# Kernel tuning notes

Measured on AMD Instinct MI355X. Metric: run time of the kernel, lower is better.

Reference implementation:

```python
import jax, jax.numpy as jnp
import numpy as np

H = 16  # num heads
EPS = 1e-5


def layer_norm(x, g, b):
    mu = jnp.mean(x, axis=-1, keepdims=True)
    var = jnp.var(x, axis=-1, keepdims=True)
    return (x - mu) * jax.lax.rsqrt(var + EPS) * g + b


def setup_inputs() -> dict:
    key = jax.random.key(0)
    ks = jax.random.split(key, 8)
    B, T, D, TE = 4, 4096, 1024, 1024
    s = 0.02  # weight init scale
    return {
        "x": jax.random.normal(ks[0], (B, T, D), jnp.float32),
        "emb": jax.random.normal(ks[1], (B, 1, TE), jnp.float32),
        "gate_msa": jax.random.normal(ks[2], (B, 1, D), jnp.float32),
        "norm_g": jnp.ones((D,), jnp.float32),
        "norm_b": jnp.zeros((D,), jnp.float32),
        "Wq": jax.random.normal(ks[3], (D, D), jnp.float32) * s,
        "bq": jnp.zeros((D,), jnp.float32),
        "Wk": jax.random.normal(ks[4], (D, D), jnp.float32) * s,
        "bk": jnp.zeros((D,), jnp.float32),
        "Wv": jax.random.normal(ks[5], (D, D), jnp.float32) * s,
        "bv": jnp.zeros((D,), jnp.float32),
        "emb_W": jax.random.normal(ks[6], (TE, 2 * D), jnp.float32) * s,
        "emb_b": jnp.zeros((2 * D,), jnp.float32),
        "sn_g": jnp.ones((D,), jnp.float32),
        "sn_b": jnp.zeros((D,), jnp.float32),
        "out_W": jax.random.normal(ks[7], (D, D), jnp.float32) * s,
        "out_b": jnp.zeros((D,), jnp.float32),
    }


def reference(x, emb, gate_msa, norm_g, norm_b, Wq, bq, Wk, bk, Wv, bv,
              emb_W, emb_b, sn_g, sn_b, out_W, out_b):
    B, T, D = x.shape
    dh = D // H
    xn = layer_norm(x, norm_g, norm_b)
    q = (xn @ Wq + bq).reshape(B, T, H, dh)
    k = (xn @ Wk + bk).reshape(B, T, H, dh)
    v = (xn @ Wv + bv).reshape(B, T, H, dh)
    q = jax.nn.softmax(q, axis=-1)      # feature-dim softmax
    k = jax.nn.softmax(k, axis=1)       # temporal softmax
    ctx = jnp.einsum('bnhd,bnhl->bhdl', k, v)  # [B,H,dh,dh] context
    y = jnp.einsum('bnhd,bhdl->bnhl', q, ctx).reshape(B, T, D)
    # StylizationBlock (dropout=0 eval semantics)
    emb_out = jax.nn.silu(emb) @ emb_W + emb_b        # [B,1,2D]
    scale, shift = jnp.split(emb_out, 2, axis=-1)
    h = layer_norm(y, sn_g, sn_b) * (1.0 + scale) + shift
    h = jax.nn.silu(h) @ out_W + out_b
    return x + gate_msa * h
```

## Files before the change

kernel.cpp:

```cpp
#include <hip/hip_runtime.h>
#include <stdint.h>

typedef unsigned short u16;
typedef float f32x4 __attribute__((ext_vector_type(4)));
typedef __bf16 bf16x8 __attribute__((ext_vector_type(8)));

__device__ __forceinline__ float b2f(u16 u) {
    union { unsigned int i; float f; } w; w.i = ((unsigned int)u) << 16; return w.f;
}
__device__ __forceinline__ u16 f2b(float f) {
    union { float f; unsigned int i; } w; w.f = f;
    unsigned int r = w.i + 0x7fffu + ((w.i >> 16) & 1u);
    return (u16)(r >> 16);
}
__device__ __forceinline__ void gload16(const void* g, void* l) {
    __builtin_amdgcn_global_load_lds(
        (const __attribute__((address_space(1))) unsigned int*)g,
        (__attribute__((address_space(3))) unsigned int*)l, 16, 0, 0);
}

__global__ __launch_bounds__(256) void prep_k(
    const float* __restrict__ Wq, const float* __restrict__ Wk, const float* __restrict__ Wv,
    const float* __restrict__ Wo, const float* __restrict__ bq, const float* __restrict__ bk,
    const float* __restrict__ bv, const float* __restrict__ ob,
    u16* __restrict__ WqkvT, u16* __restrict__ WoT, float* __restrict__ biasAll,
    float* __restrict__ zeroBase)
{
    int bz = blockIdx.x, tid = threadIdx.x;
    if (bz < 4096) {
        int z = bz >> 10, rem = bz & 1023;
        const float* src = (z == 0) ? Wq : (z == 1) ? Wk : (z == 2) ? Wv : Wo;
        u16* dst = (z < 3) ? (WqkvT + (size_t)z * 1024 * 1024) : WoT;
        __shared__ u16 tile[32][33];
        int tx = tid & 31, ty = tid >> 5;
        int n0 = (rem & 31) * 32, k0 = (rem >> 5) * 32;
#pragma unroll
        for (int i = 0; i < 4; i++) tile[ty + 8 * i][tx] = f2b(src[(size_t)(k0 + ty + 8 * i) * 1024 + n0 + tx]);
        __syncthreads();
#pragma unroll
        for (int i = 0; i < 4; i++) dst[(size_t)(n0 + ty + 8 * i) * 1024 + k0 + tx] = tile[tx][ty + 8 * i];
    } else if (bz < 4112) {
        int i = (bz - 4096) * 256 + tid;
        float v;
        if (i < 1024) v = bq[i];
        else if (i < 2048) v = bk[i - 1024];
        else if (i < 3072) v = bv[i - 2048];
        else v = ob[i - 3072];
        biasAll[i] = v;
    } else {
        int e = (bz - 4112) * 256 + tid;
        ((float4*)zeroBase)[e] = make_float4(0.f, 0.f, 0.f, 0.f);
    }
}

__global__ __launch_bounds__(256) void ln_x(
    const float* __restrict__ x, const float* __restrict__ g, const float* __restrict__ bt,
    u16* __restrict__ xn)
{
    int row = blockIdx.x, tid = threadIdx.x;
    const float* xr = x + (size_t)row * 1024;
    float4 u = *(const float4*)(xr + tid * 4);
    float v0 = u.x, v1 = u.y, v2 = u.z, v3 = u.w;
    float s = v0 + v1 + v2 + v3;
    float s2 = v0 * v0 + v1 * v1 + v2 * v2 + v3 * v3;
#pragma unroll
    for (int m = 32; m > 0; m >>= 1) { s += __shfl_xor(s, m, 64); s2 += __shfl_xor(s2, m, 64); }
    __shared__ float red[8];
    int w = tid >> 6, lane = tid & 63;
    if (lane == 0) { red[w] = s; red[4 + w] = s2; }
    __syncthreads();
    s = red[0] + red[1] + red[2] + red[3];
    s2 = red[4] + red[5] + red[6] + red[7];
    float mean = s * (1.f / 1024.f);
    float var = s2 * (1.f / 1024.f) - mean * mean;
    float rstd = rsqrtf(var + 1e-5f);
    int c = tid * 4;
    float4 gg = *(const float4*)(g + c);
    float4 bb = *(const float4*)(bt + c);
    ushort4 o;
    o.x = f2b((v0 - mean) * rstd * gg.x + bb.x);
    o.y = f2b((v1 - mean) * rstd * gg.y + bb.y);
    o.z = f2b((v2 - mean) * rstd * gg.z + bb.z);
    o.w = f2b((v3 - mean) * rstd * gg.w + bb.w);
    *(ushort4*)(xn + (size_t)row * 1024 + c) = o;
}

__global__ __launch_bounds__(256) void gemm128(
    const u16* __restrict__ A, const u16* __restrict__ Bt, const float* __restrict__ bias,
    int mode, u16* __restrict__ Qb, u16* __restrict__ Kb, u16* __restrict__ Vb,
    float* __restrict__ colsum, float* __restrict__ Cf,
    const float* __restrict__ Xf, const float* __restrict__ gate)
{
    const int K = 1024;
    __shared__ __align__(16) u16 As[128 * 64];
    __shared__ __align__(16) u16 Bs[128 * 64];
    int tid = threadIdx.x, lane = tid & 63, w = tid >> 6;
    int wm = w >> 1, wn = w & 1;
    int NB = gridDim.x;
    int lid = blockIdx.y * NB + blockIdx.x;
    int xcd = lid & 7;
    int i_ = lid >> 3;
    int rowLocal = i_ & 15;
    int colIdx = i_ >> 4;
    size_t rowbase = (size_t)(xcd * 16 + rowLocal) * 128;
    size_t colbase = (size_t)colIdx * 128;
    const u16* Ab = A + rowbase * K;
    const u16* Bb = Bt + colbase * K;
    f32x4 acc[4][4] = {};
    int quad = lane >> 4, mr = lane & 15;
    int scol = (((lane & 7) ^ ((lane >> 3) & 7))) * 8;
    int srow = lane >> 3;
    int swA = mr & 7;
    for (int k0 = 0; k0 < K; k0 += 64) {
#pragma unroll
        for (int j = 0; j < 4; j++) {
            int r = w * 32 + j * 8 + srow;
            gload16(Ab + (size_t)r * K + k0 + scol, &As[(w * 32 + j * 8) * 64]);
            gload16(Bb + (size_t)r * K + k0 + scol, &Bs[(w * 32 + j * 8) * 64]);
        }
        __syncthreads();
#pragma unroll
        for (int kk = 0; kk < 64; kk += 32) {
            bf16x8 a[4], bf[4];
#pragma unroll
            for (int i = 0; i < 4; i++)
                a[i] = *(const bf16x8*)&As[(wm * 64 + i * 16 + mr) * 64 + ((((kk >> 3) + quad) ^ swA) * 8)];
#pragma unroll
            for (int j = 0; j < 4; j++)
                bf[j] = *(const bf16x8*)&Bs[(wn * 64 + j * 16 + mr) * 64 + ((((kk >> 3) + quad) ^ swA) * 8)];
#pragma unroll
            for (int i = 0; i < 4; i++)
#pragma unroll
                for (int j = 0; j < 4; j++)
                    acc[i][j] = __builtin_amdgcn_mfma_f32_16x16x32_bf16(a[i], bf[j], acc[i][j], 0, 0, 0);
        }
        __syncthreads();
    }
    int colj[4]; float bj[4];
#pragma unroll
    for (int j = 0; j < 4; j++) { colj[j] = (int)colbase + wn * 64 + j * 16 + mr; bj[j] = bias[colj[j]]; }
    int creg = (int)colbase + wn * 64;
    if (mode == 0) {
        if (creg < 1024) {
#pragma unroll
            for (int i = 0; i < 4; i++) {
#pragma unroll
                for (int r = 0; r < 4; r++) {
                    size_t row = rowbase + wm * 64 + i * 16 + quad * 4 + r;
                    float v[4], m = -1e30f, ss = 0.f;
#pragma unroll
                    for (int j = 0; j < 4; j++) { v[j] = acc[i][j][r] + bj[j]; m = fmaxf(m, v[j]); }
#pragma unroll
                    for (int s = 1; s < 16; s <<= 1) m = fmaxf(m, __shfl_xor(m, s, 64));
#pragma unroll
                    for (int j = 0; j < 4; j++) { v[j] = __expf(v[j] - m); ss += v[j]; }
#pragma unroll
                    for (int s = 1; s < 16; s <<= 1) ss += __shfl_xor(ss, s, 64);
                    float inv = 1.f / ss;
#pragma unroll
                    for (int j = 0; j < 4; j++) Qb[row * 1024 + colj[j]] = f2b(v[j] * inv);
                }
            }
        } else if (creg < 2048) {
            int b_ = (int)(rowbase >> 12);
            float csum[4] = {};
#pragma unroll
            for (int j = 0; j < 4; j++) {
#pragma unroll
                for (int i = 0; i < 4; i++) {
#pragma unroll
                    for (int r = 0; r < 4; r++) {
                        size_t row = rowbase + wm * 64 + i * 16 + quad * 4 + r;
                        float e = __expf(acc[i][j][r] + bj[j]);
                        Kb[row * 1024 + (colj[j] - 1024)] = f2b(e);
                        csum[j] += e;
                    }
                }
            }
#pragma unroll
            for (int j = 0; j < 4; j++) {
                csum[j] += __shfl_xor(csum[j], 16, 64);
                csum[j] += __shfl_xor(csum[j], 32, 64);
                if (quad == 0) atomicAdd(&colsum[b_ * 1024 + (colj[j] - 1024)], csum[j]);
            }
        } else {
#pragma unroll
            for (int j = 0; j < 4; j++) {
#pragma unroll
                for (int i = 0; i < 4; i++) {
#pragma unroll
                    for (int r = 0; r < 4; r++) {
                        size_t row = rowbase + wm * 64 + i * 16 + quad * 4 + r;
                        Vb[row * 1024 + (colj[j] - 2048)] = f2b(acc[i][j][r] + bj[j]);
                    }
                }
            }
        }
        return;
    }
    int b_ = (int)(rowbase >> 12);
#pragma unroll
    for (int j = 0; j < 4; j++) {
        float gv = gate[b_ * 1024 + colj[j]];
#pragma unroll
        for (int i = 0; i < 4; i++) {
#pragma unroll
            for (int r = 0; r < 4; r++) {
                size_t row = rowbase + wm * 64 + i * 16 + quad * 4 + r;
                float v = acc[i][j][r] + bj[j];
                Cf[row * 1024 + colj[j]] = Xf[row * 1024 + colj[j]] + gv * v;
            }
        }
    }
}

__global__ __launch_bounds__(256) void ctx_k(
    const u16* __restrict__ kbuf, const u16* __restrict__ vbuf,
    const float* __restrict__ colsum, float* __restrict__ ctx)
{
    int ch = blockIdx.x, h = blockIdx.y, b = blockIdx.z;
    __shared__ __align__(16) float Es[16][64];
    __shared__ __align__(16) float Vs[16][64];
    int tid = threadIdx.x;
    int td = tid >> 4, tl = tid & 15;
    float invc = 1.f / colsum[b * 1024 + h * 64 + (tid & 63)];
    float acc[4][4] = {};
    size_t rowbase = (size_t)b * 4096 + ch * 512;
    for (int g = 0; g < 32; ++g) {
#pragma unroll
        for (int rep = 0; rep < 4; ++rep) {
            int e = tid + rep * 256;
            int r = e >> 6, cc = e & 63;
            size_t base = (rowbase + g * 16 + r) * 1024 + h * 64 + cc;
            Es[r][cc] = b2f(kbuf[base]) * invc;
            Vs[r][cc] = b2f(vbuf[base]);
        }
        __syncthreads();
#pragma unroll
        for (int n = 0; n < 16; n++) {
            f32x4 e4 = *(const f32x4*)&Es[n][td * 4];
            f32x4 v4 = *(const f32x4*)&Vs[n][tl * 4];
#pragma unroll
            for (int i = 0; i < 4; i++)
#pragma unroll
                for (int j = 0; j < 4; j++) acc[i][j] += e4[i] * v4[j];
        }
        __syncthreads();
    }
    float* cb = ctx + (size_t)(b * 16 + h) * 4096;
#pragma unroll
    for (int i = 0; i < 4; i++)
#pragma unroll
        for (int j = 0; j < 4; j++)
            atomicAdd(&cb[(td * 4 + i) * 64 + tl * 4 + j], acc[i][j]);
}

__global__ __launch_bounds__(256) void embout_k(
    const float* __restrict__ emb, const float* __restrict__ embW, float* __restrict__ eo)
{
    int cb = blockIdx.x, kc = blockIdx.y;
    __shared__ float semb[512];
    int tid = threadIdx.x;
#pragma unroll
    for (int i = 0; i < 2; i++) {
        int e = tid + i * 256;
        int b = e >> 7, kk = e & 127;
        float xv = emb[b * 1024 + kc * 128 + kk];
        semb[e] = xv / (1.f + __expf(-xv));
    }
    __syncthreads();
    int o = cb * 256 + tid;
    float a0 = 0, a1 = 0, a2 = 0, a3 = 0;
    for (int kk = 0; kk < 128; kk++) {
        float wv = embW[(size_t)(kc * 128 + kk) * 2048 + o];
        a0 += semb[kk] * wv; a1 += semb[128 + kk] * wv;
        a2 += semb[256 + kk] * wv; a3 += semb[384 + kk] * wv;
    }
    atomicAdd(&eo[o], a0);
    atomicAdd(&eo[2048 + o], a1);
    atomicAdd(&eo[4096 + o], a2);
    atomicAdd(&eo[6144 + o], a3);
}

__global__ __launch_bounds__(256) void y_k(
    const u16* __restrict__ q, const float* __restrict__ ctx, u16* __restrict__ y)
{
    int mc = blockIdx.x, h = blockIdx.y, b = blockIdx.z;
    __shared__ __align__(16) u16 Qs[128 * 64];
    __shared__ __align__(16) u16 Cs[64 * 72];
    int tid = threadIdx.x, lane = tid & 63, w = tid >> 6;
    size_t row0 = (size_t)b * 4096 + (size_t)mc * 128;
    const u16* Qb = q + row0 * 1024 + h * 64;
    int sr = tid >> 3, g_ = tid & 7;
    int scb = (g_ ^ (sr & 7)) * 8;
#pragma unroll
    for (int p = 0; p < 4; p++) {
        int r = p * 32 + sr;
        *(uint4*)&Qs[r * 64 + scb] = *(const uint4*)&Qb[(size_t)r * 1024 + g_ * 8];
    }
    const float* Cb = ctx + (size_t)(b * 16 + h) * 4096;
#pragma unroll
    for (int rep = 0; rep < 16; ++rep) {
        int e = tid + rep * 256;
        int d = e >> 6, l = e & 63;
        Cs[l * 72 + d] = f2b(Cb[e]);
    }
    __syncthreads();
    int quad = lane >> 4, mr = lane & 15;
    int swA = mr & 7;
    f32x4 acc[2][4] = {};
#pragma unroll
    for (int kk = 0; kk < 64; kk += 32) {
        bf16x8 a[2], bb[4];
#pragma unroll
        for (int i = 0; i < 2; i++)
            a[i] = *(const bf16x8*)&Qs[(w * 32 + i * 16 + mr) * 64 + ((((kk >> 3) + quad) ^ swA) * 8)];
#pragma unroll
        for (int j = 0; j < 4; j++) bb[j] = *(const bf16x8*)&Cs[(j * 16 + mr) * 72 + kk + quad * 8];
#pragma unroll
        for (int i = 0; i < 2; i++)
#pragma unroll
            for (int j = 0; j < 4; j++)
                acc[i][j] = __builtin_amdgcn_mfma_f32_16x16x32_bf16(a[i], bb[j], acc[i][j], 0, 0, 0);
    }
#pragma unroll
    for (int i = 0; i < 2; i++)
#pragma unroll
        for (int j = 0; j < 4; j++)
#pragma unroll
            for (int r = 0; r < 4; r++) {
                size_t row = row0 + w * 32 + i * 16 + quad * 4 + r;
                int col = h * 64 + j * 16 + mr;
                y[row * 1024 + col] = f2b(acc[i][j][r]);
            }
}

__global__ __launch_bounds__(256) void style_k(
    u16* __restrict__ y, const float* __restrict__ eo, const float* __restrict__ embb,
    const float* __restrict__ sng, const float* __restrict__ snb)
{
    int row = blockIdx.x, tid = threadIdx.x, b = row >> 12;
    u16* yr = y + (size_t)row * 1024;
    ushort4 u = *(const ushort4*)(yr + tid * 4);
    float vv[4] = { b2f(u.x), b2f(u.y), b2f(u.z), b2f(u.w) };
    float s = vv[0] + vv[1] + vv[2] + vv[3];
    float s2 = vv[0] * vv[0] + vv[1] * vv[1] + vv[2] * vv[2] + vv[3] * vv[3];
#pragma unroll
    for (int m = 32; m > 0; m >>= 1) { s += __shfl_xor(s, m, 64); s2 += __shfl_xor(s2, m, 64); }
    __shared__ float red[8];
    int w = tid >> 6, lane = tid & 63;
    if (lane == 0) { red[w] = s; red[4 + w] = s2; }
    __syncthreads();
    s = red[0] + red[1] + red[2] + red[3];
    s2 = red[4] + red[5] + red[6] + red[7];
    float mean = s * (1.f / 1024.f);
    float var = s2 * (1.f / 1024.f) - mean * mean;
    float rstd = rsqrtf(var + 1e-5f);
    int c = tid * 4;
    ushort4 o;
    u16* op = (u16*)&o;
#pragma unroll
    for (int i = 0; i < 4; i++) {
        int cc = c + i;
        float scale = eo[b * 2048 + cc] + embb[cc];
        float shift = eo[b * 2048 + 1024 + cc] + embb[1024 + cc];
        float hn = (vv[i] - mean) * rstd * sng[cc] + snb[cc];
        float hh = hn * (1.f + scale) + shift;
        op[i] = f2b(hh / (1.f + __expf(-hh)));
    }
    *(ushort4*)(yr + c) = o;
}

extern "C" void kernel_launch(void* const* d_in, const int* in_sizes, int n_in,
                              void* d_out, int out_size, void* d_ws, size_t ws_size,
                              hipStream_t stream)
{
    const float* x    = (const float*)d_in[0];
    const float* emb  = (const float*)d_in[1];
    const float* gate = (const float*)d_in[2];
    const float* ng   = (const float*)d_in[3];
    const float* nb   = (const float*)d_in[4];
    const float* Wq   = (const float*)d_in[5];
    const float* bq   = (const float*)d_in[6];
    const float* Wk   = (const float*)d_in[7];
    const float* bk   = (const float*)d_in[8];
    const float* Wv   = (const float*)d_in[9];
    const float* bv   = (const float*)d_in[10];
    const float* embW = (const float*)d_in[11];
    const float* embB = (const float*)d_in[12];
    const float* sng  = (const float*)d_in[13];
    const float* snb  = (const float*)d_in[14];
    const float* Wo   = (const float*)d_in[15];
    const float* ob   = (const float*)d_in[16];
    float* out = (float*)d_out;

    uint8_t* ws = (uint8_t*)d_ws;
    size_t off = 0;
    auto alloc = [&](size_t bytes) { void* p = ws + off; off += (bytes + 255) & ~(size_t)255; return p; };
    u16*   WqkvT   = (u16*)alloc(3072ull * 1024 * 2);
    u16*   WoT     = (u16*)alloc(1024ull * 1024 * 2);
    float* biasAll = (float*)alloc(4096 * 4);
    float* colsum  = (float*)alloc(4096 * 4);
    float* ctx     = (float*)alloc(64ull * 64 * 64 * 4);
    float* embout  = (float*)alloc(4ull * 2048 * 4);
    u16*   XN      = (u16*)alloc(16384ull * 1024 * 2);
    u16*   BUF0    = (u16*)alloc(16384ull * 1024 * 2);
    u16*   BUF1    = (u16*)alloc(16384ull * 1024 * 2);
    u16*   BUF2    = (u16*)alloc(16384ull * 1024 * 2);

    prep_k<<<4380, 256, 0, stream>>>(Wq, Wk, Wv, Wo, bq, bk, bv, ob, WqkvT, WoT, biasAll, colsum);
    ln_x<<<16384, 256, 0, stream>>>(x, ng, nb, XN);
    gemm128<<<dim3(24, 128), 256, 0, stream>>>(XN, WqkvT, biasAll, 0,
                                               BUF0, BUF1, BUF2, colsum, nullptr, nullptr, nullptr);
    ctx_k<<<dim3(8, 16, 4), 256, 0, stream>>>(BUF1, BUF2, colsum, ctx);
    embout_k<<<dim3(8, 8), 256, 0, stream>>>(emb, embW, embout);
    y_k<<<dim3(32, 16, 4), 256, 0, stream>>>(BUF0, ctx, XN);
    style_k<<<16384, 256, 0, stream>>>(XN, embout, embB, sng, snb);
    gemm128<<<dim3(8, 128), 256, 0, stream>>>(XN, WoT, biasAll + 3072, 2,
                                              nullptr, nullptr, nullptr, nullptr, out, x, gate);
}
```

Before: 471.2 us.

## Switch GEMMs to 256x256 tiles with double-buffered LDS pipeline; vectorize ctx and embout

Replaces the 128x128 GEMM with a 256x256-tile, 512-thread kernel. The new kernel double-buffers A/B tiles in LDS and interleaves global-to-LDS loads with MFMA quadrants under explicit barriers, vmcnt waits and s_setprio. This targets exposed load latency and raises arithmetic reuse per tile, at the cost of 128KB of LDS and heavy register use, and fewer blocks in flight. The ctx kernel now loads K/V as ushort4 vectors, and the embedding projection is split into more blocks over K for more parallelism.

Result: faster. 453.6 us (-3.7%).

```diff
diff --git a/kernel.cpp b/kernel.cpp
--- a/kernel.cpp
+++ b/kernel.cpp
@@ -85,57 +85,114 @@
     *(ushort4*)(xn + (size_t)row * 1024 + c) = o;
 }
 
-__global__ __launch_bounds__(256) void gemm128(
+__global__ __launch_bounds__(512, 2) void gemm256(
     const u16* __restrict__ A, const u16* __restrict__ Bt, const float* __restrict__ bias,
     int mode, u16* __restrict__ Qb, u16* __restrict__ Kb, u16* __restrict__ Vb,
     float* __restrict__ colsum, float* __restrict__ Cf,
     const float* __restrict__ Xf, const float* __restrict__ gate)
 {
     const int K = 1024;
-    __shared__ __align__(16) u16 As[128 * 64];
-    __shared__ __align__(16) u16 Bs[128 * 64];
+    __shared__ __align__(16) u16 L[2][2][256 * 64];
     int tid = threadIdx.x, lane = tid & 63, w = tid >> 6;
-    int wm = w >> 1, wn = w & 1;
+    int wm = w >> 2, wn = w & 3;
     int NB = gridDim.x;
     int lid = blockIdx.y * NB + blockIdx.x;
     int xcd = lid & 7;
     int i_ = lid >> 3;
-    int rowLocal = i_ & 15;
-    int colIdx = i_ >> 4;
-    size_t rowbase = (size_t)(xcd * 16 + rowLocal) * 128;
-    size_t colbase = (size_t)colIdx * 128;
+    int rowLocal = i_ & 7;
+    int colIdx = i_ >> 3;
+    size_t rowbase = (size_t)(xcd * 8 + rowLocal) * 256;
+    size_t colbase = (size_t)colIdx * 256;
     const u16* Ab = A + rowbase * K;
     const u16* Bb = Bt + colbase * K;
-    f32x4 acc[4][4] = {};
-    int quad = lane >> 4, mr = lane & 15;
-    int scol = (((lane & 7) ^ ((lane >> 3) & 7))) * 8;
+    f32x4 acc[8][4] = {};
+    int quad = lane >> 4, mr = lane & 15, swK = mr & 7;
     int srow = lane >> 3;
-    int swA = mr & 7;
-    for (int k0 = 0; k0 < K; k0 += 64) {
-#pragma unroll
-        for (int j = 0; j < 4; j++) {
-            int r = w * 32 + j * 8 + srow;
-            gload16(Ab + (size_t)r * K + k0 + scol, &As[(w * 32 + j * 8) * 64]);
-            gload16(Bb + (size_t)r * K + k0 + scol, &Bs[(w * 32 + j * 8) * 64]);
-        }
-        __syncthreads();
-#pragma unroll
-        for (int kk = 0; kk < 64; kk += 32) {
-            bf16x8 a[4], bf[4];
-#pragma unroll
-            for (int i = 0; i < 4; i++)
-                a[i] = *(const bf16x8*)&As[(wm * 64 + i * 16 + mr) * 64 + ((((kk >> 3) + quad) ^ swA) * 8)];
-#pragma unroll
-            for (int j = 0; j < 4; j++)
-                bf[j] = *(const bf16x8*)&Bs[(wn * 64 + j * 16 + mr) * 64 + ((((kk >> 3) + quad) ^ swA) * 8)];
-#pragma unroll
-            for (int i = 0; i < 4; i++)
-#pragma unroll
-                for (int j = 0; j < 4; j++)
-                    acc[i][j] = __builtin_amdgcn_mfma_f32_16x16x32_bf16(a[i], bf[j], acc[i][j], 0, 0, 0);
-        }
-        __syncthreads();
-    }
+    int scol = ((lane & 7) ^ srow) * 8;
+    u16* A0 = L[0][0]; u16* B0 = L[0][1]; u16* A1 = L[1][0]; u16* B1 = L[1][1];
+
+#define STAGE(ldsmat, gbase, hf, k0) do { \
+    _Pragma("unroll") \
+    for (int r_ = 0; r_ < 2; r_++) { \
+        int rb_ = (hf) * 128 + r_ * 64 + w * 8; \
+        gload16((gbase) + (size_t)(rb_ + srow) * 1024 + (k0) + scol, (ldsmat) + rb_ * 64); \
+    } } while (0)
+
+#define LDA(dst, src, mh) do { \
+    _Pragma("unroll") \
+    for (int i2_ = 0; i2_ < 4; i2_++) \
+    _Pragma("unroll") \
+    for (int kq_ = 0; kq_ < 2; kq_++) \
+        dst[i2_ * 2 + kq_] = *(const bf16x8*)&(src)[(wm * 128 + (mh) * 64 + i2_ * 16 + mr) * 64 + (((kq_ * 4 + quad) ^ swK) * 8)]; \
+    } while (0)
+
+#define LDB(dst, src, nh) do { \
+    _Pragma("unroll") \
+    for (int j_ = 0; j_ < 2; j_++) \
+    _Pragma("unroll") \
+    for (int kq_ = 0; kq_ < 2; kq_++) \
+        dst[j_ * 2 + kq_] = *(const bf16x8*)&(src)[(wn * 64 + (nh) * 32 + j_ * 16 + mr) * 64 + (((kq_ * 4 + quad) ^ swK) * 8)]; \
+    } while (0)
+
+#define MM(mh, nh, av, bv) do { \
+    __builtin_amdgcn_s_setprio(1); \
+    _Pragma("unroll") \
+    for (int i2_ = 0; i2_ < 4; i2_++) \
+    _Pragma("unroll") \
+    for (int j_ = 0; j_ < 2; j_++) \
+    _Pragma("unroll") \
+    for (int kq_ = 0; kq_ < 2; kq_++) \
+        acc[(mh) * 4 + i2_][(nh) * 2 + j_] = __builtin_amdgcn_mfma_f32_16x16x32_bf16( \
+            av[i2_ * 2 + kq_], bv[j_ * 2 + kq_], acc[(mh) * 4 + i2_][(nh) * 2 + j_], 0, 0, 0); \
+    __builtin_amdgcn_s_setprio(0); } while (0)
+
+#define BAR() asm volatile("s_barrier" ::: "memory")
+#define VMW(n) asm volatile("s_waitcnt vmcnt(" #n ")" ::: "memory")
+
+    STAGE(A0, Ab, 0, 0); STAGE(A0, Ab, 1, 0);
+    STAGE(B0, Bb, 0, 0); STAGE(B0, Bb, 1, 0);
+    STAGE(B1, Bb, 0, 64); STAGE(B1, Bb, 1, 64);
+    VMW(4);
+    BAR();
+
+    bf16x8 a[8], bn0[4], bn1[4];
+    for (int t = 0; t < 8; ++t) {
+        int k0 = t * 128;
+        bool last = (t == 7);
+        LDA(a, A0, 0); LDB(bn0, B0, 0);
+        STAGE(A1, Ab, 0, k0 + 64);
+        BAR(); MM(0, 0, a, bn0); BAR();
+        LDB(bn1, B0, 1);
+        STAGE(A1, Ab, 1, k0 + 64);
+        BAR(); MM(0, 1, a, bn1); BAR();
+        LDA(a, A0, 1);
+        if (!last) STAGE(B0, Bb, 0, k0 + 128);
+        BAR(); MM(1, 1, a, bn1); BAR();
+        if (!last) STAGE(B0, Bb, 1, k0 + 128);
+        BAR(); MM(1, 0, a, bn0);
+        if (last) { VMW(0); } else { VMW(4); }
+        BAR();
+        LDA(a, A1, 0); LDB(bn0, B1, 0);
+        if (!last) STAGE(A0, Ab, 0, k0 + 128);
+        BAR(); MM(0, 0, a, bn0); BAR();
+        LDB(bn1, B1, 1);
+        if (!last) STAGE(A0, Ab, 1, k0 + 128);
+        BAR(); MM(0, 1, a, bn1); BAR();
+        LDA(a, A1, 1);
+        if (!last) STAGE(B1, Bb, 0, k0 + 192);
+        BAR(); MM(1, 1, a, bn1); BAR();
+        if (!last) STAGE(B1, Bb, 1, k0 + 192);
+        BAR(); MM(1, 0, a, bn0);
+        if (!last) VMW(4);
+        BAR();
+    }
+#undef STAGE
+#undef LDA
+#undef LDB
+#undef MM
+#undef BAR
+#undef VMW
+
     int colj[4]; float bj[4];
 #pragma unroll
     for (int j = 0; j < 4; j++) { colj[j] = (int)colbase + wn * 64 + j * 16 + mr; bj[j] = bias[colj[j]]; }
@@ -143,10 +200,10 @@
     if (mode == 0) {
         if (creg < 1024) {
 #pragma unroll
-            for (int i = 0; i < 4; i++) {
+            for (int i = 0; i < 8; i++) {
 #pragma unroll
                 for (int r = 0; r < 4; r++) {
-                    size_t row = rowbase + wm * 64 + i * 16 + quad * 4 + r;
+                    size_t row = rowbase + wm * 128 + i * 16 + quad * 4 + r;
                     float v[4], m = -1e30f, ss = 0.f;
 #pragma unroll
                     for (int j = 0; j < 4; j++) { v[j] = acc[i][j][r] + bj[j]; m = fmaxf(m, v[j]); }
@@ -167,10 +224,10 @@
 #pragma unroll
             for (int j = 0; j < 4; j++) {
 #pragma unroll
-                for (int i = 0; i < 4; i++) {
+                for (int i = 0; i < 8; i++) {
 #pragma unroll
                     for (int r = 0; r < 4; r++) {
-                        size_t row = rowbase + wm * 64 + i * 16 + quad * 4 + r;
+                        size_t row = rowbase + wm * 128 + i * 16 + quad * 4 + r;
                         float e = __expf(acc[i][j][r] + bj[j]);
                         Kb[row * 1024 + (colj[j] - 1024)] = f2b(e);
                         csum[j] += e;
@@ -187,10 +244,10 @@
 #pragma unroll
             for (int j = 0; j < 4; j++) {
 #pragma unroll
-                for (int i = 0; i < 4; i++) {
+                for (int i = 0; i < 8; i++) {
 #pragma unroll
                     for (int r = 0; r < 4; r++) {
-                        size_t row = rowbase + wm * 64 + i * 16 + quad * 4 + r;
+                        size_t row = rowbase + wm * 128 + i * 16 + quad * 4 + r;
                         Vb[row * 1024 + (colj[j] - 2048)] = f2b(acc[i][j][r] + bj[j]);
                     }
                 }
@@ -203,10 +260,10 @@
     for (int j = 0; j < 4; j++) {
         float gv = gate[b_ * 1024 + colj[j]];
 #pragma unroll
-        for (int i = 0; i < 4; i++) {
+        for (int i = 0; i < 8; i++) {
 #pragma unroll
             for (int r = 0; r < 4; r++) {
-                size_t row = rowbase + wm * 64 + i * 16 + quad * 4 + r;
+                size_t row = rowbase + wm * 128 + i * 16 + quad * 4 + r;
                 float v = acc[i][j][r] + bj[j];
                 Cf[row * 1024 + colj[j]] = Xf[row * 1024 + colj[j]] + gv * v;
             }
@@ -223,18 +280,18 @@
     __shared__ __align__(16) float Vs[16][64];
     int tid = threadIdx.x;
     int td = tid >> 4, tl = tid & 15;
-    float invc = 1.f / colsum[b * 1024 + h * 64 + (tid & 63)];
+    int lr = tid >> 4, lc = (tid & 15) * 4;
+    const float* cs = colsum + b * 1024 + h * 64 + lc;
+    float4 inv4 = make_float4(1.f / cs[0], 1.f / cs[1], 1.f / cs[2], 1.f / cs[3]);
     float acc[4][4] = {};
     size_t rowbase = (size_t)b * 4096 + ch * 512;
     for (int g = 0; g < 32; ++g) {
-#pragma unroll
-        for (int rep = 0; rep < 4; ++rep) {
-            int e = tid + rep * 256;
-            int r = e >> 6, cc = e & 63;
-            size_t base = (rowbase + g * 16 + r) * 1024 + h * 64 + cc;
-            Es[r][cc] = b2f(kbuf[base]) * invc;
-            Vs[r][cc] = b2f(vbuf[base]);
-        }
+        size_t base = (rowbase + g * 16 + lr) * 1024 + h * 64 + lc;
+        ushort4 kv = *(const ushort4*)&kbuf[base];
+        ushort4 vv = *(const ushort4*)&vbuf[base];
+        *(float4*)&Es[lr][lc] = make_float4(b2f(kv.x) * inv4.x, b2f(kv.y) * inv4.y,
+                                            b2f(kv.z) * inv4.z, b2f(kv.w) * inv4.w);
+        *(float4*)&Vs[lr][lc] = make_float4(b2f(vv.x), b2f(vv.y), b2f(vv.z), b2f(vv.w));
         __syncthreads();
 #pragma unroll
         for (int n = 0; n < 16; n++) {
@@ -259,22 +316,20 @@
     const float* __restrict__ emb, const float* __restrict__ embW, float* __restrict__ eo)
 {
     int cb = blockIdx.x, kc = blockIdx.y;
-    __shared__ float semb[512];
+    __shared__ float semb[128];
     int tid = threadIdx.x;
-#pragma unroll
-    for (int i = 0; i < 2; i++) {
-        int e = tid + i * 256;
-        int b = e >> 7, kk = e & 127;
-        float xv = emb[b * 1024 + kc * 128 + kk];
-        semb[e] = xv / (1.f + __expf(-xv));
+    if (tid < 128) {
+        int b = tid >> 5, kk = tid & 31;
+        float xv = emb[b * 1024 + kc * 32 + kk];
+        semb[tid] = xv / (1.f + __expf(-xv));
     }
     __syncthreads();
     int o = cb * 256 + tid;
     float a0 = 0, a1 = 0, a2 = 0, a3 = 0;
-    for (int kk = 0; kk < 128; kk++) {
-        float wv = embW[(size_t)(kc * 128 + kk) * 2048 + o];
-        a0 += semb[kk] * wv; a1 += semb[128 + kk] * wv;
-        a2 += semb[256 + kk] * wv; a3 += semb[384 + kk] * wv;
+    for (int kk = 0; kk < 32; kk++) {
+        float wv = embW[(size_t)(kc * 32 + kk) * 2048 + o];
+        a0 += semb[kk] * wv; a1 += semb[32 + kk] * wv;
+        a2 += semb[64 + kk] * wv; a3 += semb[96 + kk] * wv;
     }
     atomicAdd(&eo[o], a0);
     atomicAdd(&eo[2048 + o], a1);
@@ -410,12 +465,12 @@
 
     prep_k<<<4380, 256, 0, stream>>>(Wq, Wk, Wv, Wo, bq, bk, bv, ob, WqkvT, WoT, biasAll, colsum);
     ln_x<<<16384, 256, 0, stream>>>(x, ng, nb, XN);
-    gemm128<<<dim3(24, 128), 256, 0, stream>>>(XN, WqkvT, biasAll, 0,
-                                               BUF0, BUF1, BUF2, colsum, nullptr, nullptr, nullptr);
+    gemm256<<<dim3(12, 64), 512, 0, stream>>>(XN, WqkvT, biasAll, 0,
+                                              BUF0, BUF1, BUF2, colsum, nullptr, nullptr, nullptr);
     ctx_k<<<dim3(8, 16, 4), 256, 0, stream>>>(BUF1, BUF2, colsum, ctx);
-    embout_k<<<dim3(8, 8), 256, 0, stream>>>(emb, embW, embout);
+    embout_k<<<dim3(8, 32), 256, 0, stream>>>(emb, embW, embout);
     y_k<<<dim3(32, 16, 4), 256, 0, stream>>>(BUF0, ctx, XN);
     style_k<<<16384, 256, 0, stream>>>(XN, embout, embB, sng, snb);
-    gemm128<<<dim3(8, 128), 256, 0, stream>>>(XN, WoT, biasAll + 3072, 2,
-                                              nullptr, nullptr, nullptr, nullptr, out, x, gate);
-}
+    gemm256<<<dim3(4, 64), 512, 0, stream>>>(XN, WoT, biasAll + 3072, 2,
+                                             nullptr, nullptr, nullptr, nullptr, out, x, gate);
+}
```
